# Kernel tuning notes

Hardware: AMD Instinct MI355X
Metric: run time of the kernel (lower is better)

The kernel has to match this reference:

```python
import jax, jax.numpy as jnp
import numpy as np

B, H, W, D, NH = 8, 32, 32, 64, 4  # batch, spatial dims, depth (=head dim), num_heads
S = H * W


def setup_inputs() -> dict:
    key = jax.random.key(0)
    ks = jax.random.split(key, 9)
    inp = {
        'kvx': jax.random.normal(ks[0], (B, H, W, D), jnp.float32),
        'qx': jax.random.normal(ks[1], (B, H, W, D), jnp.float32),
        'pos_table': jax.random.normal(ks[2], (S, D), jnp.float32) * 0.02,
        'Wq': jax.random.normal(ks[3], (D, D * NH * 2), jnp.float32) * (1.0 / np.sqrt(D)),
        'bq': jnp.zeros((D * NH * 2,), jnp.float32),
        'Wka': jax.random.normal(ks[4], (D, D * NH), jnp.float32) * (1.0 / np.sqrt(D)),
        'bka': jnp.zeros((D * NH,), jnp.float32),
        'Wva': jax.random.normal(ks[5], (D, D * NH), jnp.float32) * (1.0 / np.sqrt(D)),
        'bva': jnp.zeros((D * NH,), jnp.float32),
        'Wksa': jax.random.normal(ks[6], (D, D * NH), jnp.float32) * (1.0 / np.sqrt(D)),
        'bksa': jnp.zeros((D * NH,), jnp.float32),
        'Wvsa': jax.random.normal(ks[7], (D, D * NH), jnp.float32) * (1.0 / np.sqrt(D)),
        'bvsa': jnp.zeros((D * NH,), jnp.float32),
        'Wo': jax.random.normal(ks[8], (D * NH * 2, D), jnp.float32) * (1.0 / np.sqrt(D * NH * 2)),
        'bo': jnp.zeros((D,), jnp.float32),
    }
    return inp


def _proj_heads(x, Wmat, b, heads):
    # x: (B,S,D) -> (B,heads,S,D)
    y = x @ Wmat + b
    return y.reshape(B, S, heads, D).transpose(0, 2, 1, 3)


def reference(kvx, qx, pos_table, Wq, bq, Wka, bka, Wva, bva, Wksa, bksa, Wvsa, bvsa, Wo, bo):
    pos = pos_table.reshape(H, W, D)
    qx_p = (qx + pos).reshape(B, S, D)
    kvx_p = (kvx + pos).reshape(B, S, D)

    q = _proj_heads(qx_p, Wq, bq, 2 * NH)          # (B, 2nh, S, D)
    ka = _proj_heads(kvx_p, Wka, bka, NH)
    va = _proj_heads(kvx_p, Wva, bva, NH)
    ksa = _proj_heads(qx_p, Wksa, bksa, NH)
    vsa = _proj_heads(qx_p, Wvsa, bvsa, NH)
    k = jnp.concatenate([ka, ksa], axis=1)          # (B, 2nh, S, D)
    v = jnp.concatenate([va, vsa], axis=1)

    scale = 1.0 / jnp.sqrt(jnp.float32(D))
    scores = jnp.einsum('bhqd,bhkd->bhqk', q, k) * scale
    attn = jax.nn.softmax(scores, axis=-1)          # (B, 2nh, S, S)
    ctx = jnp.einsum('bhqk,bhkd->bhqd', attn, v)    # (B, 2nh, S, D)

    ctx = ctx.transpose(0, 2, 1, 3).reshape(B, S, 2 * NH * D)
    out = (ctx @ Wo + bo).reshape(B, H, W, D)
    return out, attn
```

## Files before the change

kernel.cpp:

```cpp
#include <hip/hip_runtime.h>


typedef unsigned short u16;
typedef __attribute__((ext_vector_type(8))) short bf16x8;
typedef __attribute__((ext_vector_type(4))) float f32x4;
#define MFMA16(a,b,c) __builtin_amdgcn_mfma_f32_16x16x32_bf16(a,b,c,0,0,0)

__device__ __forceinline__ float b2f(u16 u){ return __uint_as_float(((unsigned)u)<<16); }
__device__ __forceinline__ u16 f2b(float f){
  unsigned u = __float_as_uint(f);
  u += 0x7FFFu + ((u>>16)&1u);
  return (u16)(u>>16);
}
__device__ __forceinline__ float ldf(const void* p, int i, int isf32){
  return isf32 ? ((const float*)p)[i] : b2f(((const u16*)p)[i]);
}

__global__ __launch_bounds__(256) void sniff_kernel(
    const u16* __restrict__ pos, int* __restrict__ flag)
{
  __shared__ float sm[256];
  const int t = threadIdx.x;
  float v = fabsf(b2f(pos[t]));
  if (!(v == v)) v = 1e30f;
  sm[t] = v;
  __syncthreads();
  for (int o = 128; o > 0; o >>= 1){
    if (t < o) sm[t] = fmaxf(sm[t], sm[t+o]);
    __syncthreads();
  }
  if (t == 0) *flag = (sm[0] > 1.0f) ? 1 : 0;
}

__global__ __launch_bounds__(192) void proj_kernel(
    const void* __restrict__ qx, const void* __restrict__ kvx,
    const void* __restrict__ pos,
    const void* __restrict__ Wq,  const void* __restrict__ bq,
    const void* __restrict__ Wka, const void* __restrict__ bka,
    const void* __restrict__ Wva, const void* __restrict__ bva,
    const void* __restrict__ Wksa,const void* __restrict__ bksa,
    const void* __restrict__ Wvsa,const void* __restrict__ bvsa,
    u16* __restrict__ qws, u16* __restrict__ kws,
    u16* __restrict__ vtws, const int* __restrict__ flag)
{
  __shared__ float xq[64], xkv[64];
  const int isf32 = *flag;
  const int r = blockIdx.x;
  const int s = r & 1023;
  const int t = threadIdx.x;
  if (t < 64)       xq[t] = ldf(qx, r*64 + t, isf32) + ldf(pos, s*64 + t, isf32);
  else if (t < 128) { int d = t - 64; xkv[d] = ldf(kvx, r*64 + d, isf32) + ldf(pos, s*64 + d, isf32); }
  __syncthreads();
  const int b = r >> 10;
  const int n0 = t * 8;
  const void *W, *bias; const float* x; int c, h, ncol, isv;
  if (n0 < 512)       { W=Wq;   bias=bq;   x=xq;  c=n0;      h=c>>6;     ncol=512; isv=0; }
  else if (n0 < 768)  { W=Wka;  bias=bka;  x=xkv; c=n0-512;  h=c>>6;     ncol=256; isv=0; }
  else if (n0 < 1024) { W=Wksa; bias=bksa; x=xq;  c=n0-768;  h=4+(c>>6); ncol=256; isv=0; }
  else if (n0 < 1280) { W=Wva;  bias=bva;  x=xkv; c=n0-1024; h=c>>6;     ncol=256; isv=1; }
  else                { W=Wvsa; bias=bvsa; x=xq;  c=n0-1280; h=4+(c>>6); ncol=256; isv=1; }

  float acc[8];
  #pragma unroll
  for (int j = 0; j < 8; j++) acc[j] = ldf(bias, c + j, isf32);

  if (isf32){
    const float* Wf = (const float*)W + c;
    #pragma unroll 4
    for (int k = 0; k < 64; k++){
      float xk = x[k];
      const float4* wp = (const float4*)(Wf + k*ncol);
      float4 w0 = wp[0], w1 = wp[1];
      acc[0] += xk*w0.x; acc[1] += xk*w0.y; acc[2] += xk*w0.z; acc[3] += xk*w0.w;
      acc[4] += xk*w1.x; acc[5] += xk*w1.y; acc[6] += xk*w1.z; acc[7] += xk*w1.w;
    }
  } else {
    const u16* Wu = (const u16*)W + c;
    #pragma unroll 4
    for (int k = 0; k < 64; k++){
      float xk = x[k];
      uint4 wv = *(const uint4*)(Wu + k*ncol);
      const u16* wh = (const u16*)&wv;
      #pragma unroll
      for (int j = 0; j < 8; j++) acc[j] += xk * b2f(wh[j]);
    }
  }

  const int bh = (b<<3) + h, d0 = c & 63;
  if (!isv){
    u16 val[8];
    #pragma unroll
    for (int j = 0; j < 8; j++) val[j] = f2b(acc[j]);
    uint4* dst = (uint4*)((n0 < 512 ? qws : kws) + (bh*1024 + s)*64 + d0);
    *dst = *(const uint4*)val;
  } else {
    #pragma unroll
    for (int j = 0; j < 8; j++)
      vtws[(bh*64 + d0 + j)*1024 + s] = f2b(acc[j]);
  }
}

__global__ __launch_bounds__(512, 2) void attn_kernel(
    const u16* __restrict__ qws, const u16* __restrict__ kws,
    const u16* __restrict__ vtws,
    void* __restrict__ d_out, float* __restrict__ ctx,
    const int* __restrict__ flag)
{
  __shared__ u16 sK [2][64*72];
  __shared__ u16 sVT[2][64*72];
  __shared__ u16 sP [8][16*72];

  const int isf32 = *flag;
  const int t    = threadIdx.x;
  const int w    = t >> 6;
  const int lane = t & 63;
  const int L15  = lane & 15;
  const int quad = lane >> 4;
  const int bh   = blockIdx.y;
  const int q0   = blockIdx.x * 128;
  const int qw   = q0 + w*16;

  const u16* kg = kws  + bh*65536;
  const u16* vg = vtws + bh*65536;

  const u16* qbase = qws + (bh*1024 + qw + L15)*64;
  const bf16x8 aq0 = *(const bf16x8*)(qbase + quad*8);
  const bf16x8 aq1 = *(const bf16x8*)(qbase + 32 + quad*8);

  const int srow = t >> 3;
  const int scol = (t & 7) * 8;

  const float SC = 0.125f;
  const float C0 = 8.0f;

  const u16* kptr = kg + srow*64 + scol;
  const u16* vptr = vg + srow*1024 + scol;

  float l_part[4] = {0.f,0.f,0.f,0.f};
  {
    uint4 kv = *(const uint4*)kptr;
    *(uint4*)(&sK[0][srow*72 + scol]) = kv;
  }
  for (int c = 0; c < 16; c++){
    __syncthreads();
    uint4 nk;
    if (c < 15) nk = *(const uint4*)(kptr + (c+1)*4096);
    const u16* sk = sK[c&1];
    #pragma unroll
    for (int tt = 0; tt < 4; tt++){
      bf16x8 b0 = *(const bf16x8*)(sk + (tt*16 + L15)*72 + quad*8);
      bf16x8 b1 = *(const bf16x8*)(sk + (tt*16 + L15)*72 + 32 + quad*8);
      f32x4 acc = {};
      acc = MFMA16(aq0, b0, acc);
      acc = MFMA16(aq1, b1, acc);
      #pragma unroll
      for (int r = 0; r < 4; r++)
        l_part[r] += __expf(acc[r]*SC - C0);
    }
    if (c < 15) *(uint4*)(&sK[(c+1)&1][srow*72 + scol]) = nk;
  }
  float linv[4];
  #pragma unroll
  for (int r = 0; r < 4; r++){
    float ls = l_part[r];
    ls += __shfl_xor(ls, 1);
    ls += __shfl_xor(ls, 2);
    ls += __shfl_xor(ls, 4);
    ls += __shfl_xor(ls, 8);
    linv[r] = 1.f / ls;
  }

  f32x4 octx[4] = {};
  u16* sPw = sP[w];
  {
    uint4 kv = *(const uint4*)kptr;
    uint4 vv = *(const uint4*)vptr;
    *(uint4*)(&sK [0][srow*72 + scol]) = kv;
    *(uint4*)(&sVT[0][srow*72 + scol]) = vv;
  }
  for (int c = 0; c < 16; c++){
    __syncthreads();
    uint4 nk, nv;
    if (c < 15){
      nk = *(const uint4*)(kptr + (c+1)*4096);
      nv = *(const uint4*)(vptr + (c+1)*64);
    }
    const u16* sk = sK[c&1];
    const u16* sv = sVT[c&1];
    #pragma unroll
    for (int tt = 0; tt < 4; tt++){
      bf16x8 b0 = *(const bf16x8*)(sk + (tt*16 + L15)*72 + quad*8);
      bf16x8 b1 = *(const bf16x8*)(sk + (tt*16 + L15)*72 + 32 + quad*8);
      f32x4 acc = {};
      acc = MFMA16(aq0, b0, acc);
      acc = MFMA16(aq1, b1, acc);
      #pragma unroll
      for (int r = 0; r < 4; r++){
        float p = __expf(acc[r]*SC - C0) * linv[r];
        sPw[(quad*4 + r)*72 + tt*16 + L15] = f2b(p);
      }
    }
    { int row = lane >> 2, cc = (lane & 3) * 16;
      const uint4* ps = (const uint4*)(sPw + row*72 + cc);
      uint4 u0 = ps[0], u1 = ps[1];
      long gofs = ((long)(bh*1024 + qw + row))*1024 + c*64 + cc;
      if (isf32){
        float* ao = (float*)d_out + 524288 + gofs;
        const u16* h0 = (const u16*)&u0; const u16* h1 = (const u16*)&u1;
        float4 f0, f1, f2, f3;
        f0.x=b2f(h0[0]); f0.y=b2f(h0[1]); f0.z=b2f(h0[2]); f0.w=b2f(h0[3]);
        f1.x=b2f(h0[4]); f1.y=b2f(h0[5]); f1.z=b2f(h0[6]); f1.w=b2f(h0[7]);
        f2.x=b2f(h1[0]); f2.y=b2f(h1[1]); f2.z=b2f(h1[2]); f2.w=b2f(h1[3]);
        f3.x=b2f(h1[4]); f3.y=b2f(h1[5]); f3.z=b2f(h1[6]); f3.w=b2f(h1[7]);
        *(float4*)(ao+0) = f0; *(float4*)(ao+4) = f1;
        *(float4*)(ao+8) = f2; *(float4*)(ao+12) = f3;
      } else {
        uint4* gd = (uint4*)((u16*)d_out + 524288 + gofs);
        gd[0] = u0; gd[1] = u1;
      }
    }
    #pragma unroll
    for (int s2 = 0; s2 < 2; s2++){
      bf16x8 ap = *(const bf16x8*)(sPw + L15*72 + s2*32 + quad*8);
      #pragma unroll
      for (int tt = 0; tt < 4; tt++){
        bf16x8 bv = *(const bf16x8*)(sv + (tt*16 + L15)*72 + s2*32 + quad*8);
        octx[tt] = MFMA16(ap, bv, octx[tt]);
      }
    }
    if (c < 15){
      *(uint4*)(&sK [(c+1)&1][srow*72 + scol]) = nk;
      *(uint4*)(&sVT[(c+1)&1][srow*72 + scol]) = nv;
    }
  }

  const int b = bh >> 3, h = bh & 7;
  #pragma unroll
  for (int tt = 0; tt < 4; tt++)
    #pragma unroll
    for (int r = 0; r < 4; r++)
      ctx[(b*1024 + qw + quad*4 + r)*512 + h*64 + tt*16 + L15] = octx[tt][r];
}

__global__ __launch_bounds__(256) void outproj_kernel(
    const float* __restrict__ ctx, const void* __restrict__ Wo,
    const void* __restrict__ bo, void* __restrict__ d_out,
    const int* __restrict__ flag)
{
  __shared__ float sctx[4*512];
  const int isf32 = *flag;
  const int t  = threadIdx.x;
  const int r0 = blockIdx.x * 4;
  #pragma unroll
  for (int j = 0; j < 8; j++){
    int i = t + 256*j;
    sctx[i] = ctx[r0*512 + i];
  }
  __syncthreads();
  const int row = t >> 6, dc = t & 63;
  float acc = ldf(bo, dc, isf32);
  if (isf32){
    const float* Wf = (const float*)Wo;
    #pragma unroll 8
    for (int c = 0; c < 512; c++) acc += sctx[row*512 + c] * Wf[c*64 + dc];
    ((float*)d_out)[(r0 + row)*64 + dc] = acc;
  } else {
    const u16* Wu = (const u16*)Wo;
    #pragma unroll 8
    for (int c = 0; c < 512; c++) acc += sctx[row*512 + c] * b2f(Wu[c*64 + dc]);
    ((u16*)d_out)[(r0 + row)*64 + dc] = f2b(acc);
  }
}

extern "C" void kernel_launch(void* const* d_in, const int* in_sizes, int n_in,
                              void* d_out, int out_size, void* d_ws, size_t ws_size,
                              hipStream_t stream)
{
  const void* kvx  = d_in[0];
  const void* qx   = d_in[1];
  const void* pos  = d_in[2];
  const void* Wq   = d_in[3];
  const void* bq   = d_in[4];
  const void* Wka  = d_in[5];
  const void* bka  = d_in[6];
  const void* Wva  = d_in[7];
  const void* bva  = d_in[8];
  const void* Wksa = d_in[9];
  const void* bksa = d_in[10];
  const void* Wvsa = d_in[11];
  const void* bvsa = d_in[12];
  const void* Wo   = d_in[13];
  const void* bo   = d_in[14];

  int* flag = (int*)d_ws;
  u16* qws  = (u16*)((char*)d_ws + 1024);
  u16* kws  = qws + 4194304;
  u16* vtws = kws + 4194304;
  float* ctx = (float*)(vtws + 4194304);

  sniff_kernel<<<dim3(1), dim3(256), 0, stream>>>((const u16*)pos, flag);
  proj_kernel<<<dim3(8192), dim3(192), 0, stream>>>(
      qx, kvx, pos, Wq, bq, Wka, bka, Wva, bva, Wksa, bksa, Wvsa, bvsa,
      qws, kws, vtws, flag);
  attn_kernel<<<dim3(8, 64), dim3(512), 0, stream>>>(qws, kws, vtws, d_out, ctx, flag);
  outproj_kernel<<<dim3(2048), dim3(256), 0, stream>>>(ctx, Wo, bo, d_out, flag);
}
```

Baseline: 554.5 us.

## Register-block projection and output-projection kernels over multiple rows

The projection kernel now handles 8 token rows per block, so each weight load is reused across 8 rows held in an 8x8 register accumulator tile, and the grid shrinks to match. The output projection kernel handles 16 rows per block with 4 rows per thread, loads ctx via float4, and reuses each Wo element across 4 rows. Both changes aim to cut redundant global weight traffic. In exchange they raise register pressure and reduce the number of blocks.

```diff
diff --git a/kernel.cpp b/kernel.cpp
--- a/kernel.cpp
+++ b/kernel.cpp
@@ -43,60 +43,87 @@
     u16* __restrict__ qws, u16* __restrict__ kws,
     u16* __restrict__ vtws, const int* __restrict__ flag)
 {
-  __shared__ float xq[64], xkv[64];
+  __shared__ float xq[8][64], xkv[8][64];
   const int isf32 = *flag;
-  const int r = blockIdx.x;
-  const int s = r & 1023;
-  const int t = threadIdx.x;
-  if (t < 64)       xq[t] = ldf(qx, r*64 + t, isf32) + ldf(pos, s*64 + t, isf32);
-  else if (t < 128) { int d = t - 64; xkv[d] = ldf(kvx, r*64 + d, isf32) + ldf(pos, s*64 + d, isf32); }
+  const int r0 = blockIdx.x * 8;
+  const int s0 = r0 & 1023;
+  const int b  = r0 >> 10;
+  const int t  = threadIdx.x;
+
+  for (int i = t; i < 1024; i += 192){
+    int row = (i >> 6) & 7, d = i & 63;
+    if (i < 512) xq [row][d] = ldf(qx,  (r0+row)*64 + d, isf32) + ldf(pos, (s0+row)*64 + d, isf32);
+    else         xkv[row][d] = ldf(kvx, (r0+row)*64 + d, isf32) + ldf(pos, (s0+row)*64 + d, isf32);
+  }
   __syncthreads();
-  const int b = r >> 10;
+
   const int n0 = t * 8;
-  const void *W, *bias; const float* x; int c, h, ncol, isv;
-  if (n0 < 512)       { W=Wq;   bias=bq;   x=xq;  c=n0;      h=c>>6;     ncol=512; isv=0; }
-  else if (n0 < 768)  { W=Wka;  bias=bka;  x=xkv; c=n0-512;  h=c>>6;     ncol=256; isv=0; }
-  else if (n0 < 1024) { W=Wksa; bias=bksa; x=xq;  c=n0-768;  h=4+(c>>6); ncol=256; isv=0; }
-  else if (n0 < 1280) { W=Wva;  bias=bva;  x=xkv; c=n0-1024; h=c>>6;     ncol=256; isv=1; }
-  else                { W=Wvsa; bias=bvsa; x=xq;  c=n0-1280; h=4+(c>>6); ncol=256; isv=1; }
-
-  float acc[8];
-  #pragma unroll
-  for (int j = 0; j < 8; j++) acc[j] = ldf(bias, c + j, isf32);
+  const void *W, *bias; int c, h, ncol, isv, useq;
+  if (n0 < 512)       { W=Wq;   bias=bq;   useq=1; c=n0;      h=c>>6;     ncol=512; isv=0; }
+  else if (n0 < 768)  { W=Wka;  bias=bka;  useq=0; c=n0-512;  h=c>>6;     ncol=256; isv=0; }
+  else if (n0 < 1024) { W=Wksa; bias=bksa; useq=1; c=n0-768;  h=4+(c>>6); ncol=256; isv=0; }
+  else if (n0 < 1280) { W=Wva;  bias=bva;  useq=0; c=n0-1024; h=c>>6;     ncol=256; isv=1; }
+  else                { W=Wvsa; bias=bvsa; useq=1; c=n0-1280; h=4+(c>>6); ncol=256; isv=1; }
+  const float (*xp)[64] = useq ? xq : xkv;
+
+  float bs[8];
+  #pragma unroll
+  for (int j = 0; j < 8; j++) bs[j] = ldf(bias, c + j, isf32);
+
+  float acc[8][8];
+  #pragma unroll
+  for (int r = 0; r < 8; r++)
+    #pragma unroll
+    for (int j = 0; j < 8; j++) acc[r][j] = bs[j];
 
   if (isf32){
     const float* Wf = (const float*)W + c;
     #pragma unroll 4
     for (int k = 0; k < 64; k++){
-      float xk = x[k];
       const float4* wp = (const float4*)(Wf + k*ncol);
       float4 w0 = wp[0], w1 = wp[1];
-      acc[0] += xk*w0.x; acc[1] += xk*w0.y; acc[2] += xk*w0.z; acc[3] += xk*w0.w;
-      acc[4] += xk*w1.x; acc[5] += xk*w1.y; acc[6] += xk*w1.z; acc[7] += xk*w1.w;
+      float wv[8] = {w0.x,w0.y,w0.z,w0.w,w1.x,w1.y,w1.z,w1.w};
+      #pragma unroll
+      for (int r = 0; r < 8; r++){
+        float xk = xp[r][k];
+        #pragma unroll
+        for (int j = 0; j < 8; j++) acc[r][j] += xk * wv[j];
+      }
     }
   } else {
     const u16* Wu = (const u16*)W + c;
     #pragma unroll 4
     for (int k = 0; k < 64; k++){
-      float xk = x[k];
-      uint4 wv = *(const uint4*)(Wu + k*ncol);
-      const u16* wh = (const u16*)&wv;
-      #pragma unroll
-      for (int j = 0; j < 8; j++) acc[j] += xk * b2f(wh[j]);
+      uint4 wvv = *(const uint4*)(Wu + k*ncol);
+      const u16* wh = (const u16*)&wvv;
+      float wv[8];
+      #pragma unroll
+      for (int j = 0; j < 8; j++) wv[j] = b2f(wh[j]);
+      #pragma unroll
+      for (int r = 0; r < 8; r++){
+        float xk = xp[r][k];
+        #pragma unroll
+        for (int j = 0; j < 8; j++) acc[r][j] += xk * wv[j];
+      }
     }
   }
 
   const int bh = (b<<3) + h, d0 = c & 63;
   if (!isv){
-    u16 val[8];
-    #pragma unroll
-    for (int j = 0; j < 8; j++) val[j] = f2b(acc[j]);
-    uint4* dst = (uint4*)((n0 < 512 ? qws : kws) + (bh*1024 + s)*64 + d0);
-    *dst = *(const uint4*)val;
+    u16* base = (n0 < 512 ? qws : kws);
+    #pragma unroll
+    for (int r = 0; r < 8; r++){
+      u16 val[8];
+      #pragma unroll
+      for (int j = 0; j < 8; j++) val[j] = f2b(acc[r][j]);
+      *(uint4*)(base + ((bh*1024 + s0 + r)*64 + d0)) = *(const uint4*)val;
+    }
   } else {
     #pragma unroll
     for (int j = 0; j < 8; j++)
-      vtws[(bh*64 + d0 + j)*1024 + s] = f2b(acc[j]);
+      #pragma unroll
+      for (int r = 0; r < 8; r++)
+        vtws[(bh*64 + d0 + j)*1024 + (s0 + r)] = f2b(acc[r][j]);
   }
 }
 
@@ -247,28 +274,43 @@
     const void* __restrict__ bo, void* __restrict__ d_out,
     const int* __restrict__ flag)
 {
-  __shared__ float sctx[4*512];
+  __shared__ float sctx[16*512];
   const int isf32 = *flag;
   const int t  = threadIdx.x;
-  const int r0 = blockIdx.x * 4;
-  #pragma unroll
-  for (int j = 0; j < 8; j++){
-    int i = t + 256*j;
-    sctx[i] = ctx[r0*512 + i];
-  }
+  const int r0 = blockIdx.x * 16;
+  { const float4* cp = (const float4*)(ctx + r0*512);
+    float4* sp = (float4*)sctx;
+    #pragma unroll
+    for (int j = 0; j < 8; j++) sp[t + 256*j] = cp[t + 256*j]; }
   __syncthreads();
-  const int row = t >> 6, dc = t & 63;
-  float acc = ldf(bo, dc, isf32);
+
+  const int dc = t & 63, rg = t >> 6;
+  float acc[4];
+  #pragma unroll
+  for (int i = 0; i < 4; i++) acc[i] = ldf(bo, dc, isf32);
+
   if (isf32){
     const float* Wf = (const float*)Wo;
     #pragma unroll 8
-    for (int c = 0; c < 512; c++) acc += sctx[row*512 + c] * Wf[c*64 + dc];
-    ((float*)d_out)[(r0 + row)*64 + dc] = acc;
+    for (int c = 0; c < 512; c++){
+      float w = Wf[c*64 + dc];
+      #pragma unroll
+      for (int i = 0; i < 4; i++) acc[i] += sctx[(rg*4 + i)*512 + c] * w;
+    }
+    #pragma unroll
+    for (int i = 0; i < 4; i++)
+      ((float*)d_out)[(r0 + rg*4 + i)*64 + dc] = acc[i];
   } else {
     const u16* Wu = (const u16*)Wo;
     #pragma unroll 8
-    for (int c = 0; c < 512; c++) acc += sctx[row*512 + c] * b2f(Wu[c*64 + dc]);
-    ((u16*)d_out)[(r0 + row)*64 + dc] = f2b(acc);
+    for (int c = 0; c < 512; c++){
+      float w = b2f(Wu[c*64 + dc]);
+      #pragma unroll
+      for (int i = 0; i < 4; i++) acc[i] += sctx[(rg*4 + i)*512 + c] * w;
+    }
+    #pragma unroll
+    for (int i = 0; i < 4; i++)
+      ((u16*)d_out)[(r0 + rg*4 + i)*64 + dc] = f2b(acc[i]);
   }
 }
 
@@ -299,9 +341,9 @@
   float* ctx = (float*)(vtws + 4194304);
 
   sniff_kernel<<<dim3(1), dim3(256), 0, stream>>>((const u16*)pos, flag);
-  proj_kernel<<<dim3(8192), dim3(192), 0, stream>>>(
+  proj_kernel<<<dim3(1024), dim3(192), 0, stream>>>(
       qx, kvx, pos, Wq, bq, Wka, bka, Wva, bva, Wksa, bksa, Wvsa, bvsa,
       qws, kws, vtws, flag);
   attn_kernel<<<dim3(8, 64), dim3(512), 0, stream>>>(qws, kws, vtws, d_out, ctx, flag);
-  outproj_kernel<<<dim3(2048), dim3(256), 0, stream>>>(ctx, Wo, bo, d_out, flag);
-}
+  outproj_kernel<<<dim3(512), dim3(256), 0, stream>>>(ctx, Wo, bo, d_out, flag);
+}
```

New measurement: 448.7 us. 19.1% less time.
